# Kernel optimization log

Measured on AMD Instinct MI355X. Metric: run time of the kernel, lower is better.

## Reference

```python
import jax, jax.numpy as jnp
import numpy as np

N_NODES = 50000
N_EDGES = 1600000
DIM = 128
SLOPE = 0.2  # LeakyReLU negative slope


def setup_inputs() -> dict:
    key = jax.random.key(0)
    ks = jax.random.split(key, 9)
    indices = jax.random.randint(ks[0], (2, N_EDGES), 0, N_NODES)
    features = jax.random.normal(ks[1], (N_NODES, DIM), dtype=jnp.float32)
    W1_w = jax.random.normal(ks[2], (DIM, DIM), dtype=jnp.float32) * 0.05
    W1_b = jax.random.normal(ks[3], (DIM,), dtype=jnp.float32) * 0.05
    W2_w = jax.random.normal(ks[4], (DIM, DIM), dtype=jnp.float32) * 0.05
    W2_b = jax.random.normal(ks[5], (DIM,), dtype=jnp.float32) * 0.05
    Watt_w = jax.random.normal(ks[6], (DIM, DIM), dtype=jnp.float32) * 0.05
    Watt_b = jax.random.normal(ks[7], (DIM,), dtype=jnp.float32) * 0.05
    a = jax.random.normal(ks[8], (2 * DIM, 1), dtype=jnp.float32) * 0.05
    return {"indices": indices, "features": features, "num_nodes": N_NODES,
            "W1_w": W1_w, "W1_b": W1_b, "W2_w": W2_w, "W2_b": W2_b,
            "Watt_w": Watt_w, "Watt_b": Watt_b, "a": a}


def reference(indices, features, num_nodes, W1_w, W1_b, W2_w, W2_b, Watt_w, Watt_b, a):
    src, dst = indices[0], indices[1]
    d = W1_w.shape[1]
    # attention scores: e_ij = leakyrelu(cat(h_src, h_dst) @ a) == h_src@a1 + h_dst@a2
    h_att = features @ Watt_w + Watt_b                      # [N, d]
    a1, a2 = a[:d], a[d:]                                    # each [d, 1]
    e = jax.nn.leaky_relu(h_att[src] @ a1 + h_att[dst] @ a2, SLOPE)  # [E, 1]
    # global-max-stabilized segment softmax over incoming edges of dst
    e = e - jnp.max(e)
    exp_e = jnp.exp(e)                                       # [E, 1]
    denom = jax.ops.segment_sum(exp_e, dst, num_segments=num_nodes)  # [N, 1]
    alpha = exp_e / (denom[dst] + 1e-9)                      # [E, 1]
    # weighted message aggregation
    h_msg = features @ W1_w + W1_b                           # [N, d]
    weighted = h_msg[src] * alpha                            # [E, d]
    h_neigh = jax.ops.segment_sum(weighted, dst, num_segments=num_nodes)  # [N, d]
    # in_dim == out_dim -> h_self = features (module skips extra W1)
    h_self = features
    sum_h = h_self + h_neigh
    prod_h = h_self * h_neigh
    return jax.nn.leaky_relu(sum_h + prod_h @ W2_w + W2_b, SLOPE)
```

## Files before the change

kernel.cpp:

```cpp
#include <hip/hip_runtime.h>

#define DIM 128
#define SLOPE 0.2f
#define NPBK 64
#define SLAB 4000
#define CHUNK_A 8192
#define EPT 32
#define KMAX 1024
#define WT_STRIDE 136

typedef __attribute__((ext_vector_type(8))) short bf16x8;
typedef __attribute__((ext_vector_type(4))) float f32x4;

__device__ __forceinline__ float leaky(float x) { return x > 0.f ? x : SLOPE * x; }

__device__ __forceinline__ unsigned short f2bf(float x) {
    unsigned u = __float_as_uint(x);
    return (unsigned short)((u + 0x7FFFu + ((u >> 16) & 1u)) >> 16);
}
__device__ __forceinline__ float bf2f(unsigned short h) {
    return __uint_as_float(((unsigned)h) << 16);
}
__device__ __forceinline__ bf16x8 pack_bf16x8(float4 a, float4 b) {
    bf16x8 r;
    r[0] = (short)f2bf(a.x); r[1] = (short)f2bf(a.y);
    r[2] = (short)f2bf(a.z); r[3] = (short)f2bf(a.w);
    r[4] = (short)f2bf(b.x); r[5] = (short)f2bf(b.y);
    r[6] = (short)f2bf(b.z); r[7] = (short)f2bf(b.w);
    return r;
}

__global__ void k_prep(const float* __restrict__ Watt_w, const float* __restrict__ Watt_b,
                       const float* __restrict__ a, float* __restrict__ v1,
                       float* __restrict__ v2, float* __restrict__ c12) {
    int k = threadIdx.x;
    __shared__ float a1s[DIM], a2s[DIM];
    __shared__ float r1[DIM], r2[DIM];
    a1s[k] = a[k];
    a2s[k] = a[DIM + k];
    __syncthreads();
    float acc1 = 0.f, acc2 = 0.f;
    const float* row = Watt_w + (size_t)k * DIM;
    for (int j = 0; j < DIM; ++j) {
        float w = row[j];
        acc1 += w * a1s[j];
        acc2 += w * a2s[j];
    }
    v1[k] = acc1;
    v2[k] = acc2;
    float b = Watt_b[k];
    r1[k] = b * a1s[k];
    r2[k] = b * a2s[k];
    __syncthreads();
    for (int off = 64; off > 0; off >>= 1) {
        if (k < off) { r1[k] += r1[k + off]; r2[k] += r2[k + off]; }
        __syncthreads();
    }
    if (k == 0) { c12[0] = r1[0]; c12[1] = r2[0]; }
}

__global__ __launch_bounds__(256) void k_fused_fwd(
    const float* __restrict__ feat, const float* __restrict__ W1,
    const float* __restrict__ W1b, const float* __restrict__ v1,
    const float* __restrict__ v2, const float* __restrict__ c12,
    unsigned short* __restrict__ h_msg, float* __restrict__ s1, float* __restrict__ s2,
    const int* __restrict__ src, const int* __restrict__ dst,
    int* __restrict__ bucket_cur, int* __restrict__ ebuf,
    int n_nodes, int n_tiles16, int n_edges, int K, int nb_part, int total_waves) {
    __shared__ union {
        struct { unsigned short Wt[DIM * WT_STRIDE]; float v1s[DIM]; float v2s[DIM]; } g;
        struct { int h[KMAX]; int lcur[KMAX]; } p;
    } sm;
    int tid = threadIdx.x;

    if (blockIdx.x < nb_part) {
        int* h = sm.p.h;
        int* lcur = sm.p.lcur;
        for (int i = tid; i < KMAX; i += 256) h[i] = 0;
        __syncthreads();
        int cbase = blockIdx.x * CHUNK_A;
        int pval[EPT], pb[EPT];
        #pragma unroll
        for (int p = 0; p < 8; ++p) {
            int i0 = cbase + p * 1024 + tid * 4;
            if (i0 + 3 < n_edges) {
                int4 d = *(const int4*)&dst[i0];
                int4 s = *(const int4*)&src[i0];
                int b0 = d.x >> 6, b1 = d.y >> 6, b2 = d.z >> 6, b3 = d.w >> 6;
                atomicAdd(&h[b0], 1); atomicAdd(&h[b1], 1);
                atomicAdd(&h[b2], 1); atomicAdd(&h[b3], 1);
                pb[p * 4 + 0] = b0; pval[p * 4 + 0] = ((d.x & 63) << 17) | s.x;
                pb[p * 4 + 1] = b1; pval[p * 4 + 1] = ((d.y & 63) << 17) | s.y;
                pb[p * 4 + 2] = b2; pval[p * 4 + 2] = ((d.z & 63) << 17) | s.z;
                pb[p * 4 + 3] = b3; pval[p * 4 + 3] = ((d.w & 63) << 17) | s.w;
            } else {
                #pragma unroll
                for (int k = 0; k < 4; ++k) {
                    int i = i0 + k;
                    if (i < n_edges) {
                        int d = dst[i], s = src[i];
                        int b = d >> 6;
                        atomicAdd(&h[b], 1);
                        pb[p * 4 + k] = b;
                        pval[p * 4 + k] = ((d & 63) << 17) | s;
                    } else {
                        pb[p * 4 + k] = -1;
                        pval[p * 4 + k] = 0;
                    }
                }
            }
        }
        __syncthreads();
        for (int i = tid; i < K; i += 256) {
            int c = h[i];
            lcur[i] = c ? (i * SLAB + atomicAdd(&bucket_cur[i], c)) : 0;
        }
        __syncthreads();
        #pragma unroll
        for (int k = 0; k < EPT; ++k) {
            int b = pb[k];
            if (b >= 0) {
                int pos = atomicAdd(&lcur[b], 1);
                ebuf[pos] = pval[k];
            }
        }
        return;
    }

    unsigned short* Wt = sm.g.Wt;
    float* v1s = sm.g.v1s;
    float* v2s = sm.g.v2s;
    for (int i = tid; i < DIM * DIM; i += 256) {
        int k = i >> 7, n = i & 127;
        Wt[n * WT_STRIDE + k] = f2bf(W1[i]);
    }
    if (tid < DIM) { v1s[tid] = v1[tid]; v2s[tid] = v2[tid]; }
    __syncthreads();

    int lane = tid & 63, wid = tid >> 6;
    int ln15 = lane & 15, q = lane >> 4;
    float c1 = c12[0], c2 = c12[1];
    float bias[8];
    #pragma unroll
    for (int nt = 0; nt < 8; ++nt) bias[nt] = W1b[nt * 16 + ln15];

    for (int t = (blockIdx.x - nb_part) * 4 + wid; t < n_tiles16; t += total_waves) {
        int base = t * 16;
        int row = base + ln15;
        bool valid = row < n_nodes;
        const float* frow = feat + (size_t)row * DIM;
        bf16x8 afr[4];
        float p1 = 0.f, p2 = 0.f;
        #pragma unroll
        for (int kc = 0; kc < 4; ++kc) {
            int col0 = kc * 32 + q * 8;
            float4 u0 = {0.f, 0.f, 0.f, 0.f}, u1 = {0.f, 0.f, 0.f, 0.f};
            if (valid) {
                u0 = *(const float4*)&frow[col0];
                u1 = *(const float4*)&frow[col0 + 4];
            }
            float4 wa = *(const float4*)&v1s[col0];
            float4 wb = *(const float4*)&v1s[col0 + 4];
            float4 wc = *(const float4*)&v2s[col0];
            float4 wd = *(const float4*)&v2s[col0 + 4];
            p1 += u0.x * wa.x + u0.y * wa.y + u0.z * wa.z + u0.w * wa.w
                + u1.x * wb.x + u1.y * wb.y + u1.z * wb.z + u1.w * wb.w;
            p2 += u0.x * wc.x + u0.y * wc.y + u0.z * wc.z + u0.w * wc.w
                + u1.x * wd.x + u1.y * wd.y + u1.z * wd.z + u1.w * wd.w;
            afr[kc] = pack_bf16x8(u0, u1);
        }
        p1 += __shfl_xor(p1, 16, 64); p1 += __shfl_xor(p1, 32, 64);
        p2 += __shfl_xor(p2, 16, 64); p2 += __shfl_xor(p2, 32, 64);
        if (q == 0 && valid) { s1[row] = p1 + c1; s2[row] = p2 + c2; }

        f32x4 acc[8];
        #pragma unroll
        for (int nt = 0; nt < 8; ++nt)
            acc[nt] = (f32x4){bias[nt], bias[nt], bias[nt], bias[nt]};
        #pragma unroll
        for (int kc = 0; kc < 4; ++kc) {
            #pragma unroll
            for (int nt = 0; nt < 8; ++nt) {
                bf16x8 b = *(const bf16x8*)&Wt[(nt * 16 + ln15) * WT_STRIDE + kc * 32 + q * 8];
                acc[nt] = __builtin_amdgcn_mfma_f32_16x16x32_bf16(afr[kc], b, acc[nt], 0, 0, 0);
            }
        }
        #pragma unroll
        for (int nt = 0; nt < 8; ++nt) {
            #pragma unroll
            for (int r = 0; r < 4; ++r) {
                int rr = base + q * 4 + r;
                if (rr < n_nodes)
                    h_msg[(size_t)rr * DIM + nt * 16 + ln15] = f2bf(acc[nt][r]);
            }
        }
    }
}

__global__ __launch_bounds__(256) void k_bcsr(const int* __restrict__ ebuf,
                                              const int* __restrict__ bucket_cur,
                                              int* __restrict__ row,
                                              unsigned short* __restrict__ csr_src,
                                              int n_nodes, int K) {
    __shared__ int bins[NPBK], scn[NPBK], cur[NPBK];
    int b = blockIdx.x;
    int tid = threadIdx.x;
    int start = b * SLAB;
    int end = start + bucket_cur[b];
    if (tid < NPBK) bins[tid] = 0;
    __syncthreads();
    for (int i = start + tid; i < end; i += 256)
        atomicAdd(&bins[ebuf[i] >> 17], 1);
    __syncthreads();
    if (tid < NPBK) scn[tid] = bins[tid];
    __syncthreads();
    for (int off = 1; off < NPBK; off <<= 1) {
        int v = (tid < NPBK && tid >= off) ? scn[tid - off] : 0;
        __syncthreads();
        if (tid < NPBK) scn[tid] += v;
        __syncthreads();
    }
    if (tid < NPBK) {
        int node = b * NPBK + tid;
        if (node < n_nodes) row[node] = start + scn[tid];
        cur[tid] = start + scn[tid] - bins[tid];
    }
    __syncthreads();
    for (int i = start + tid; i < end; i += 256) {
        int v = ebuf[i];
        int pos = atomicAdd(&cur[v >> 17], 1);
        csr_src[pos] = (unsigned short)(v & 0xFFFF);
    }
}

__global__ __launch_bounds__(256) void k_gather(
    const int* __restrict__ row, const unsigned short* __restrict__ csr_src,
    const float* __restrict__ s1, const float* __restrict__ s2,
    const unsigned short* __restrict__ h_msg, float* __restrict__ h_neigh, int n_nodes) {
    int g = (blockIdx.x * blockDim.x + threadIdx.x) >> 5;
    if (g >= n_nodes) return;
    int lane = threadIdx.x & 31;
    int begin = ((g & (NPBK - 1)) == 0) ? (g >> 6) * SLAB : row[g - 1];
    int end = row[g];
    float s2d = s2[g];
    float4 accA = {0.f, 0.f, 0.f, 0.f}, accB = {0.f, 0.f, 0.f, 0.f};
    float wA = 0.f, wB = 0.f;
    int j = begin;
    int iA = (j < end) ? (int)csr_src[j] : 0;
    int iB = (j + 1 < end) ? (int)csr_src[j + 1] : 0;
    float pA = s1[iA], pB = s1[iB];
    while (j + 1 < end) {
        int cA = iA, cB = iB;
        float sA = pA, sB = pB;
        int jn = j + 2;
        if (jn < end)     iA = (int)csr_src[jn];
        if (jn + 1 < end) iB = (int)csr_src[jn + 1];
        pA = s1[iA]; pB = s1[iB];
        ushort4 uA = *(const ushort4*)&h_msg[(size_t)cA * DIM + lane * 4];
        ushort4 uB = *(const ushort4*)&h_msg[(size_t)cB * DIM + lane * 4];
        float eA = __expf(leaky(sA + s2d));
        float eB = __expf(leaky(sB + s2d));
        accA.x += eA * bf2f(uA.x); accA.y += eA * bf2f(uA.y);
        accA.z += eA * bf2f(uA.z); accA.w += eA * bf2f(uA.w);
        wA += eA;
        accB.x += eB * bf2f(uB.x); accB.y += eB * bf2f(uB.y);
        accB.z += eB * bf2f(uB.z); accB.w += eB * bf2f(uB.w);
        wB += eB;
        j = jn;
    }
    if (j < end) {
        int cA = iA;
        ushort4 uA = *(const ushort4*)&h_msg[(size_t)cA * DIM + lane * 4];
        float eA = __expf(leaky(pA + s2d));
        accA.x += eA * bf2f(uA.x); accA.y += eA * bf2f(uA.y);
        accA.z += eA * bf2f(uA.z); accA.w += eA * bf2f(uA.w);
        wA += eA;
    }
    float wsum = wA + wB;
    float inv = 1.f / (wsum + 1e-9f);
    float4 o;
    o.x = (accA.x + accB.x) * inv;
    o.y = (accA.y + accB.y) * inv;
    o.z = (accA.z + accB.z) * inv;
    o.w = (accA.w + accB.w) * inv;
    *(float4*)&h_neigh[(size_t)g * DIM + lane * 4] = o;
}

__global__ __launch_bounds__(256) void k_final(
    const float* __restrict__ feat, const float* __restrict__ h_neigh,
    const float* __restrict__ W2, const float* __restrict__ W2b,
    float* __restrict__ out, int n_nodes, int n_tiles16, int total_waves) {
    __shared__ unsigned short Wt[DIM * WT_STRIDE];
    int tid = threadIdx.x;
    for (int i = tid; i < DIM * DIM; i += 256) {
        int k = i >> 7, n = i & 127;
        Wt[n * WT_STRIDE + k] = f2bf(W2[i]);
    }
    __syncthreads();

    int lane = tid & 63, wid = tid >> 6;
    int ln15 = lane & 15, q = lane >> 4;
    float bias[8];
    #pragma unroll
    for (int nt = 0; nt < 8; ++nt) bias[nt] = W2b[nt * 16 + ln15];

    for (int t = blockIdx.x * 4 + wid; t < n_tiles16; t += total_waves) {
        int base = t * 16;
        int row = base + ln15;
        bool valid = row < n_nodes;
        const float* frow = feat + (size_t)row * DIM;
        const float* hrow = h_neigh + (size_t)row * DIM;
        bf16x8 afr[4];
        #pragma unroll
        for (int kc = 0; kc < 4; ++kc) {
            int col0 = kc * 32 + q * 8;
            float4 p0 = {0.f, 0.f, 0.f, 0.f}, p1 = {0.f, 0.f, 0.f, 0.f};
            if (valid) {
                float4 f0 = *(const float4*)&frow[col0];
                float4 f1 = *(const float4*)&frow[col0 + 4];
                float4 h0 = *(const float4*)&hrow[col0];
                float4 h1 = *(const float4*)&hrow[col0 + 4];
                p0.x = f0.x * h0.x; p0.y = f0.y * h0.y;
                p0.z = f0.z * h0.z; p0.w = f0.w * h0.w;
                p1.x = f1.x * h1.x; p1.y = f1.y * h1.y;
                p1.z = f1.z * h1.z; p1.w = f1.w * h1.w;
            }
            afr[kc] = pack_bf16x8(p0, p1);
        }
        f32x4 acc[8];
        #pragma unroll
        for (int nt = 0; nt < 8; ++nt)
            acc[nt] = (f32x4){bias[nt], bias[nt], bias[nt], bias[nt]};
        #pragma unroll
        for (int kc = 0; kc < 4; ++kc) {
            #pragma unroll
            for (int nt = 0; nt < 8; ++nt) {
                bf16x8 b = *(const bf16x8*)&Wt[(nt * 16 + ln15) * WT_STRIDE + kc * 32 + q * 8];
                acc[nt] = __builtin_amdgcn_mfma_f32_16x16x32_bf16(afr[kc], b, acc[nt], 0, 0, 0);
            }
        }
        #pragma unroll
        for (int r = 0; r < 4; ++r) {
            int rr = base + q * 4 + r;
            if (rr < n_nodes) {
                #pragma unroll
                for (int nt = 0; nt < 8; ++nt) {
                    int col = nt * 16 + ln15;
                    float f = feat[(size_t)rr * DIM + col];
                    float hn = h_neigh[(size_t)rr * DIM + col];
                    out[(size_t)rr * DIM + col] = leaky(f + hn + acc[nt][r]);
                }
            }
        }
    }
}

extern "C" void kernel_launch(void* const* d_in, const int* in_sizes, int n_in,
                              void* d_out, int out_size, void* d_ws, size_t ws_size,
                              hipStream_t stream) {
    const int*   indices = (const int*)d_in[0];
    const float* feat    = (const float*)d_in[1];
    const float* W1w  = (const float*)d_in[3];
    const float* W1b  = (const float*)d_in[4];
    const float* W2w  = (const float*)d_in[5];
    const float* W2b  = (const float*)d_in[6];
    const float* Wattw = (const float*)d_in[7];
    const float* Wattb = (const float*)d_in[8];
    const float* a     = (const float*)d_in[9];

    int n_edges = in_sizes[0] / 2;
    int n_nodes = in_sizes[1] / DIM;
    int n_tiles16 = (n_nodes + 15) / 16;
    int K = (n_nodes + NPBK - 1) / NPBK;
    const int* src = indices;
    const int* dst = indices + n_edges;

    unsigned short* h_msg = (unsigned short*)d_out;
    int* ebuf = (int*)(h_msg + (size_t)n_nodes * DIM);

    float* ws      = (float*)d_ws;
    float* h_neigh = ws;
    unsigned short* csr_src = (unsigned short*)(h_neigh + (size_t)n_nodes * DIM);
    int*   row     = (int*)(csr_src + (size_t)K * SLAB);
    float* s1      = (float*)(row + n_nodes);
    float* s2      = s1 + n_nodes;
    float* v1      = s2 + n_nodes;
    float* v2      = v1 + DIM;
    float* c12     = v2 + DIM;
    int*   bucket_cur = (int*)(c12 + 2);

    hipMemsetAsync(bucket_cur, 0, (size_t)KMAX * sizeof(int), stream);

    k_prep<<<1, 128, 0, stream>>>(Wattw, Wattb, a, v1, v2, c12);
    {
        int nb_part = (n_edges + CHUNK_A - 1) / CHUNK_A;
        int gemm_blocks = 512;
        k_fused_fwd<<<nb_part + gemm_blocks, 256, 0, stream>>>(
            feat, W1w, W1b, v1, v2, c12, h_msg, s1, s2,
            src, dst, bucket_cur, ebuf,
            n_nodes, n_tiles16, n_edges, K, nb_part, gemm_blocks * 4);
    }
    k_bcsr<<<K, 256, 0, stream>>>(ebuf, bucket_cur, row, csr_src, n_nodes, K);
    {
        long long threads = (long long)n_nodes * 32;
        int blocks = (int)((threads + 255) / 256);
        k_gather<<<blocks, 256, 0, stream>>>(row, csr_src, s1, s2,
                                             h_msg, h_neigh, n_nodes);
    }
    {
        int blocks = 512;
        k_final<<<blocks, 256, 0, stream>>>(feat, h_neigh, W2w, W2b,
                                            (float*)d_out, n_nodes,
                                            n_tiles16, blocks * 4);
    }
}
```

Measured before the change: 217.6 us.

## Fuse bucket CSR build, gather aggregation and output GEMM into one block-per-bucket kernel

Replaces the three back-end kernels (bucket CSR build, per-node gather, final MFMA GEMM) with a single kernel where each 1024-thread block owns one 64-node bucket. The bucket is sorted in shared memory, neighbours are aggregated by dynamically scheduled 32-lane groups into a bf16 LDS tile, and the W2 GEMM plus epilogue runs straight from that tile. This removes the global csr_src/row/h_neigh round trips and two launches. In exchange, every block re-converts W2 into LDS, the LDS footprint is large (about 60KB) which limits occupancy, and h_neigh is rounded to bf16 before the epilogue add.

Measured after the change: 216.1 us. Within noise of the previous version (-0.7%).

```diff
diff --git a/kernel.cpp b/kernel.cpp
--- a/kernel.cpp
+++ b/kernel.cpp
@@ -197,160 +197,165 @@
     }
 }
 
-__global__ __launch_bounds__(256) void k_bcsr(const int* __restrict__ ebuf,
-                                              const int* __restrict__ bucket_cur,
-                                              int* __restrict__ row,
-                                              unsigned short* __restrict__ csr_src,
-                                              int n_nodes, int K) {
-    __shared__ int bins[NPBK], scn[NPBK], cur[NPBK];
+__global__ __launch_bounds__(1024, 8) void k_back(
+    const int* __restrict__ ebuf, const int* __restrict__ bucket_cur,
+    const float* __restrict__ s1, const float* __restrict__ s2,
+    const unsigned short* __restrict__ h_msg, const float* __restrict__ feat,
+    const float* __restrict__ W2, const float* __restrict__ W2b,
+    float* __restrict__ out, int n_nodes, int K) {
+    __shared__ unsigned short Wt[DIM * WT_STRIDE];
+    __shared__ unsigned short sorted_s[SLAB];
+    __shared__ unsigned short tile_hn[NPBK * DIM];
+    __shared__ int bins[NPBK], scn_[NPBK], cur[NPBK];
+    __shared__ int next_node;
+
+    int tid = threadIdx.x;
     int b = blockIdx.x;
-    int tid = threadIdx.x;
+    int base_node = b * NPBK;
     int start = b * SLAB;
-    int end = start + bucket_cur[b];
-    if (tid < NPBK) bins[tid] = 0;
-    __syncthreads();
-    for (int i = start + tid; i < end; i += 256)
-        atomicAdd(&bins[ebuf[i] >> 17], 1);
-    __syncthreads();
-    if (tid < NPBK) scn[tid] = bins[tid];
-    __syncthreads();
-    for (int off = 1; off < NPBK; off <<= 1) {
-        int v = (tid < NPBK && tid >= off) ? scn[tid - off] : 0;
-        __syncthreads();
-        if (tid < NPBK) scn[tid] += v;
-        __syncthreads();
-    }
-    if (tid < NPBK) {
-        int node = b * NPBK + tid;
-        if (node < n_nodes) row[node] = start + scn[tid];
-        cur[tid] = start + scn[tid] - bins[tid];
-    }
-    __syncthreads();
-    for (int i = start + tid; i < end; i += 256) {
-        int v = ebuf[i];
-        int pos = atomicAdd(&cur[v >> 17], 1);
-        csr_src[pos] = (unsigned short)(v & 0xFFFF);
-    }
-}
-
-__global__ __launch_bounds__(256) void k_gather(
-    const int* __restrict__ row, const unsigned short* __restrict__ csr_src,
-    const float* __restrict__ s1, const float* __restrict__ s2,
-    const unsigned short* __restrict__ h_msg, float* __restrict__ h_neigh, int n_nodes) {
-    int g = (blockIdx.x * blockDim.x + threadIdx.x) >> 5;
-    if (g >= n_nodes) return;
-    int lane = threadIdx.x & 31;
-    int begin = ((g & (NPBK - 1)) == 0) ? (g >> 6) * SLAB : row[g - 1];
-    int end = row[g];
-    float s2d = s2[g];
-    float4 accA = {0.f, 0.f, 0.f, 0.f}, accB = {0.f, 0.f, 0.f, 0.f};
-    float wA = 0.f, wB = 0.f;
-    int j = begin;
-    int iA = (j < end) ? (int)csr_src[j] : 0;
-    int iB = (j + 1 < end) ? (int)csr_src[j + 1] : 0;
-    float pA = s1[iA], pB = s1[iB];
-    while (j + 1 < end) {
-        int cA = iA, cB = iB;
-        float sA = pA, sB = pB;
-        int jn = j + 2;
-        if (jn < end)     iA = (int)csr_src[jn];
-        if (jn + 1 < end) iB = (int)csr_src[jn + 1];
-        pA = s1[iA]; pB = s1[iB];
-        ushort4 uA = *(const ushort4*)&h_msg[(size_t)cA * DIM + lane * 4];
-        ushort4 uB = *(const ushort4*)&h_msg[(size_t)cB * DIM + lane * 4];
-        float eA = __expf(leaky(sA + s2d));
-        float eB = __expf(leaky(sB + s2d));
-        accA.x += eA * bf2f(uA.x); accA.y += eA * bf2f(uA.y);
-        accA.z += eA * bf2f(uA.z); accA.w += eA * bf2f(uA.w);
-        wA += eA;
-        accB.x += eB * bf2f(uB.x); accB.y += eB * bf2f(uB.y);
-        accB.z += eB * bf2f(uB.z); accB.w += eB * bf2f(uB.w);
-        wB += eB;
-        j = jn;
-    }
-    if (j < end) {
-        int cA = iA;
-        ushort4 uA = *(const ushort4*)&h_msg[(size_t)cA * DIM + lane * 4];
-        float eA = __expf(leaky(pA + s2d));
-        accA.x += eA * bf2f(uA.x); accA.y += eA * bf2f(uA.y);
-        accA.z += eA * bf2f(uA.z); accA.w += eA * bf2f(uA.w);
-        wA += eA;
-    }
-    float wsum = wA + wB;
-    float inv = 1.f / (wsum + 1e-9f);
-    float4 o;
-    o.x = (accA.x + accB.x) * inv;
-    o.y = (accA.y + accB.y) * inv;
-    o.z = (accA.z + accB.z) * inv;
-    o.w = (accA.w + accB.w) * inv;
-    *(float4*)&h_neigh[(size_t)g * DIM + lane * 4] = o;
-}
-
-__global__ __launch_bounds__(256) void k_final(
-    const float* __restrict__ feat, const float* __restrict__ h_neigh,
-    const float* __restrict__ W2, const float* __restrict__ W2b,
-    float* __restrict__ out, int n_nodes, int n_tiles16, int total_waves) {
-    __shared__ unsigned short Wt[DIM * WT_STRIDE];
-    int tid = threadIdx.x;
-    for (int i = tid; i < DIM * DIM; i += 256) {
+    int cnt = bucket_cur[b];
+
+    for (int i = tid; i < DIM * DIM; i += 1024) {
         int k = i >> 7, n = i & 127;
         Wt[n * WT_STRIDE + k] = f2bf(W2[i]);
     }
-    __syncthreads();
-
-    int lane = tid & 63, wid = tid >> 6;
-    int ln15 = lane & 15, q = lane >> 4;
-    float bias[8];
+    if (tid < NPBK) bins[tid] = 0;
+    if (tid == 0) next_node = 0;
+    __syncthreads();
+
+    for (int i = tid; i < cnt; i += 1024)
+        atomicAdd(&bins[((unsigned)ebuf[start + i]) >> 17], 1);
+    __syncthreads();
+    if (tid < NPBK) scn_[tid] = bins[tid];
+    __syncthreads();
+    for (int off = 1; off < NPBK; off <<= 1) {
+        int v = (tid < NPBK && tid >= off) ? scn_[tid - off] : 0;
+        __syncthreads();
+        if (tid < NPBK) scn_[tid] += v;
+        __syncthreads();
+    }
+    if (tid < NPBK) cur[tid] = scn_[tid] - bins[tid];
+    __syncthreads();
+    for (int i = tid; i < cnt; i += 1024) {
+        int v = ebuf[start + i];
+        int p = atomicAdd(&cur[v >> 17], 1);
+        sorted_s[p] = (unsigned short)(v & 0xFFFF);
+    }
+    __syncthreads();
+
+    int lane = tid & 31;
+    while (true) {
+        int g_local;
+        if (lane == 0) g_local = atomicAdd(&next_node, 1);
+        g_local = __shfl(g_local, 0, 32);
+        if (g_local >= NPBK) break;
+        int g = base_node + g_local;
+        if (g >= n_nodes) {
+            *(ushort4*)&tile_hn[g_local * DIM + lane * 4] = (ushort4){0, 0, 0, 0};
+            continue;
+        }
+        int begin = scn_[g_local] - bins[g_local];
+        int end = scn_[g_local];
+        float s2d = s2[g];
+        float4 accA = {0.f, 0.f, 0.f, 0.f}, accB = {0.f, 0.f, 0.f, 0.f};
+        float wA = 0.f, wB = 0.f;
+        int j = begin;
+        int iA = (j < end) ? (int)sorted_s[j] : 0;
+        int iB = (j + 1 < end) ? (int)sorted_s[j + 1] : 0;
+        float pA = s1[iA], pB = s1[iB];
+        while (j + 1 < end) {
+            int cA = iA, cB = iB;
+            float sA = pA, sB = pB;
+            int jn = j + 2;
+            if (jn < end)     iA = (int)sorted_s[jn];
+            if (jn + 1 < end) iB = (int)sorted_s[jn + 1];
+            pA = s1[iA]; pB = s1[iB];
+            ushort4 uA = *(const ushort4*)&h_msg[(size_t)cA * DIM + lane * 4];
+            ushort4 uB = *(const ushort4*)&h_msg[(size_t)cB * DIM + lane * 4];
+            float eA = __expf(leaky(sA + s2d));
+            float eB = __expf(leaky(sB + s2d));
+            accA.x += eA * bf2f(uA.x); accA.y += eA * bf2f(uA.y);
+            accA.z += eA * bf2f(uA.z); accA.w += eA * bf2f(uA.w);
+            wA += eA;
+            accB.x += eB * bf2f(uB.x); accB.y += eB * bf2f(uB.y);
+            accB.z += eB * bf2f(uB.z); accB.w += eB * bf2f(uB.w);
+            wB += eB;
+            j = jn;
+        }
+        if (j < end) {
+            int cA = iA;
+            ushort4 uA = *(const ushort4*)&h_msg[(size_t)cA * DIM + lane * 4];
+            float eA = __expf(leaky(pA + s2d));
+            accA.x += eA * bf2f(uA.x); accA.y += eA * bf2f(uA.y);
+            accA.z += eA * bf2f(uA.z); accA.w += eA * bf2f(uA.w);
+            wA += eA;
+        }
+        float inv = 1.f / (wA + wB + 1e-9f);
+        ushort4 o;
+        o.x = f2bf((accA.x + accB.x) * inv);
+        o.y = f2bf((accA.y + accB.y) * inv);
+        o.z = f2bf((accA.z + accB.z) * inv);
+        o.w = f2bf((accA.w + accB.w) * inv);
+        *(ushort4*)&tile_hn[g_local * DIM + lane * 4] = o;
+    }
+    __syncthreads();
+
+    int w = tid >> 6;
+    int lane64 = tid & 63;
+    int ln15 = lane64 & 15, q = lane64 >> 4;
+    int tile = w >> 2;
+    int nt0 = (w & 3) * 2;
+    int lrow = tile * 16 + ln15;
+    int grow = base_node + lrow;
+    bool valid = grow < n_nodes;
+    const float* frow = feat + (size_t)grow * DIM;
+    bf16x8 afr[4];
     #pragma unroll
-    for (int nt = 0; nt < 8; ++nt) bias[nt] = W2b[nt * 16 + ln15];
-
-    for (int t = blockIdx.x * 4 + wid; t < n_tiles16; t += total_waves) {
-        int base = t * 16;
-        int row = base + ln15;
-        bool valid = row < n_nodes;
-        const float* frow = feat + (size_t)row * DIM;
-        const float* hrow = h_neigh + (size_t)row * DIM;
-        bf16x8 afr[4];
-        #pragma unroll
-        for (int kc = 0; kc < 4; ++kc) {
-            int col0 = kc * 32 + q * 8;
-            float4 p0 = {0.f, 0.f, 0.f, 0.f}, p1 = {0.f, 0.f, 0.f, 0.f};
-            if (valid) {
-                float4 f0 = *(const float4*)&frow[col0];
-                float4 f1 = *(const float4*)&frow[col0 + 4];
-                float4 h0 = *(const float4*)&hrow[col0];
-                float4 h1 = *(const float4*)&hrow[col0 + 4];
-                p0.x = f0.x * h0.x; p0.y = f0.y * h0.y;
-                p0.z = f0.z * h0.z; p0.w = f0.w * h0.w;
-                p1.x = f1.x * h1.x; p1.y = f1.y * h1.y;
-                p1.z = f1.z * h1.z; p1.w = f1.w * h1.w;
-            }
-            afr[kc] = pack_bf16x8(p0, p1);
-        }
-        f32x4 acc[8];
-        #pragma unroll
-        for (int nt = 0; nt < 8; ++nt)
-            acc[nt] = (f32x4){bias[nt], bias[nt], bias[nt], bias[nt]};
-        #pragma unroll
-        for (int kc = 0; kc < 4; ++kc) {
-            #pragma unroll
-            for (int nt = 0; nt < 8; ++nt) {
-                bf16x8 b = *(const bf16x8*)&Wt[(nt * 16 + ln15) * WT_STRIDE + kc * 32 + q * 8];
-                acc[nt] = __builtin_amdgcn_mfma_f32_16x16x32_bf16(afr[kc], b, acc[nt], 0, 0, 0);
-            }
-        }
-        #pragma unroll
-        for (int r = 0; r < 4; ++r) {
-            int rr = base + q * 4 + r;
-            if (rr < n_nodes) {
-                #pragma unroll
-                for (int nt = 0; nt < 8; ++nt) {
-                    int col = nt * 16 + ln15;
-                    float f = feat[(size_t)rr * DIM + col];
-                    float hn = h_neigh[(size_t)rr * DIM + col];
-                    out[(size_t)rr * DIM + col] = leaky(f + hn + acc[nt][r]);
-                }
-            }
+    for (int kc = 0; kc < 4; ++kc) {
+        int col0 = kc * 32 + q * 8;
+        float4 p0 = {0.f, 0.f, 0.f, 0.f}, p1 = {0.f, 0.f, 0.f, 0.f};
+        bf16x8 hn8 = *(const bf16x8*)&tile_hn[lrow * DIM + col0];
+        if (valid) {
+            float4 f0 = *(const float4*)&frow[col0];
+            float4 f1 = *(const float4*)&frow[col0 + 4];
+            p0.x = f0.x * bf2f((unsigned short)hn8[0]);
+            p0.y = f0.y * bf2f((unsigned short)hn8[1]);
+            p0.z = f0.z * bf2f((unsigned short)hn8[2]);
+            p0.w = f0.w * bf2f((unsigned short)hn8[3]);
+            p1.x = f1.x * bf2f((unsigned short)hn8[4]);
+            p1.y = f1.y * bf2f((unsigned short)hn8[5]);
+            p1.z = f1.z * bf2f((unsigned short)hn8[6]);
+            p1.w = f1.w * bf2f((unsigned short)hn8[7]);
+        }
+        afr[kc] = pack_bf16x8(p0, p1);
+    }
+    f32x4 acc0, acc1;
+    {
+        float b0 = W2b[(nt0 + 0) * 16 + ln15];
+        float b1 = W2b[(nt0 + 1) * 16 + ln15];
+        acc0 = (f32x4){b0, b0, b0, b0};
+        acc1 = (f32x4){b1, b1, b1, b1};
+    }
+    #pragma unroll
+    for (int kc = 0; kc < 4; ++kc) {
+        bf16x8 w0 = *(const bf16x8*)&Wt[((nt0 + 0) * 16 + ln15) * WT_STRIDE + kc * 32 + q * 8];
+        bf16x8 w1 = *(const bf16x8*)&Wt[((nt0 + 1) * 16 + ln15) * WT_STRIDE + kc * 32 + q * 8];
+        acc0 = __builtin_amdgcn_mfma_f32_16x16x32_bf16(afr[kc], w0, acc0, 0, 0, 0);
+        acc1 = __builtin_amdgcn_mfma_f32_16x16x32_bf16(afr[kc], w1, acc1, 0, 0, 0);
+    }
+    #pragma unroll
+    for (int r = 0; r < 4; ++r) {
+        int rl = tile * 16 + q * 4 + r;
+        int rr = base_node + rl;
+        if (rr < n_nodes) {
+            int colA = (nt0 + 0) * 16 + ln15;
+            int colB = (nt0 + 1) * 16 + ln15;
+            float fA = feat[(size_t)rr * DIM + colA];
+            float fB = feat[(size_t)rr * DIM + colB];
+            float hA = bf2f(tile_hn[rl * DIM + colA]);
+            float hB = bf2f(tile_hn[rl * DIM + colB]);
+            out[(size_t)rr * DIM + colA] = leaky(fA + hA + acc0[r]);
+            out[(size_t)rr * DIM + colB] = leaky(fB + hB + acc1[r]);
         }
     }
 }
@@ -375,14 +380,10 @@
     const int* src = indices;
     const int* dst = indices + n_edges;
 
-    unsigned short* h_msg = (unsigned short*)d_out;
-    int* ebuf = (int*)(h_msg + (size_t)n_nodes * DIM);
-
     float* ws      = (float*)d_ws;
-    float* h_neigh = ws;
-    unsigned short* csr_src = (unsigned short*)(h_neigh + (size_t)n_nodes * DIM);
-    int*   row     = (int*)(csr_src + (size_t)K * SLAB);
-    float* s1      = (float*)(row + n_nodes);
+    unsigned short* h_msg = (unsigned short*)ws;
+    int*   ebuf    = (int*)(h_msg + (size_t)n_nodes * DIM);
+    float* s1      = (float*)(ebuf + (size_t)K * SLAB);
     float* s2      = s1 + n_nodes;
     float* v1      = s2 + n_nodes;
     float* v2      = v1 + DIM;
@@ -400,17 +401,6 @@
             src, dst, bucket_cur, ebuf,
             n_nodes, n_tiles16, n_edges, K, nb_part, gemm_blocks * 4);
     }
-    k_bcsr<<<K, 256, 0, stream>>>(ebuf, bucket_cur, row, csr_src, n_nodes, K);
-    {
-        long long threads = (long long)n_nodes * 32;
-        int blocks = (int)((threads + 255) / 256);
-        k_gather<<<blocks, 256, 0, stream>>>(row, csr_src, s1, s2,
-                                             h_msg, h_neigh, n_nodes);
-    }
-    {
-        int blocks = 512;
-        k_final<<<blocks, 256, 0, stream>>>(feat, h_neigh, W2w, W2b,
-                                            (float*)d_out, n_nodes,
-                                            n_tiles16, blocks * 4);
-    }
-}
+    k_back<<<K, 1024, 0, stream>>>(ebuf, bucket_cur, s1, s2, h_msg, feat,
+                                   W2w, W2b, (float*)d_out, n_nodes, K);
+}
```
